# Kernel tuning notes

Measured on AMD Instinct MI355X. Metric: run time of the kernel, lower is better.

## Reference

```python
import jax, jax.numpy as jnp
import numpy as np

B, P, N, E, H, D = 64, 256, 1000, 128, 8, 16
SQRT_E = 11.313708498984761  # sqrt(embedding_dim)
CLIP = 10.0                  # logit_clipping


def setup_inputs() -> dict:
    key = jax.random.key(0)
    ks = jax.random.split(key, 9)
    s = 0.05  # weight init scale
    return {
        "encoded_nodes": jax.random.normal(ks[0], (B, N, E), jnp.float32),
        "encoded_last_node": jax.random.normal(ks[1], (B, P, E), jnp.float32),
        "attr": jax.random.uniform(ks[2], (B, P, 1), jnp.float32),
        "ninf_mask": jnp.zeros((B, P, N), jnp.float32),
        # params stored [in, out] (apply as x @ W, equals torch Linear with W.T)
        "Wq_last": jax.random.normal(ks[3], (E + 1, H * D), jnp.float32) * s,
        "Wk": jax.random.normal(ks[4], (E, H * D), jnp.float32) * s,
        "Wv": jax.random.normal(ks[5], (E, H * D), jnp.float32) * s,
        "Wo": jax.random.normal(ks[6], (H * D, E), jnp.float32) * s,
        "bo": jax.random.normal(ks[7], (E,), jnp.float32) * s,
    }


def reference(encoded_nodes, encoded_last_node, attr, ninf_mask,
              Wq_last, Wk, Wv, Wo, bo):
    # set_kv: project encoded nodes to per-head K, V  -> [B, N, H, D]
    k = (encoded_nodes @ Wk).reshape(B, N, H, D)
    v = (encoded_nodes @ Wv).reshape(B, N, H, D)

    # query from (last node embedding, attr) -> [B, P, H, D]
    input_cat = jnp.concatenate([encoded_last_node, attr], axis=2)  # [B,P,E+1]
    q = (input_cat @ Wq_last).reshape(B, P, H, D)

    # multi-head attention with additive rank-3 -inf mask
    inv_sqrt_d = 1.0 / jnp.sqrt(jnp.float32(D))
    scores = jnp.einsum("bphd,bnhd->bhpn", q, k) * inv_sqrt_d
    scores = scores + ninf_mask[:, None, :, :]            # [B,H,P,N]
    weights = jax.nn.softmax(scores, axis=-1)
    out = jnp.einsum("bhpn,bnhd->bphd", weights, v).reshape(B, P, H * D)

    mh = out @ Wo + bo                                    # [B,P,E]

    # single-head tanh-clipped scoring against encoded nodes
    score = jnp.einsum("bpe,bne->bpn", mh, encoded_nodes) / SQRT_E
    score_masked = CLIP * jnp.tanh(score) + ninf_mask
    probs = jax.nn.softmax(score_masked, axis=2)          # [B,P,N]
    return probs
```

## Files before the change

### kernel.cpp

```cpp
#include <hip/hip_runtime.h>

#define BB 64
#define PP 256
#define NN 1000
#define NP 1024
#define EE 128
#define HH 8
#define DD 16

typedef __fp16 v4h __attribute__((ext_vector_type(4)));
typedef float v4f __attribute__((ext_vector_type(4)));


__global__ __launch_bounds__(256) void k1_qproj(const float* __restrict__ ln,
                                                const float* __restrict__ attr,
                                                const float* __restrict__ Wq,
                                                __fp16* __restrict__ Qh) {
    __shared__ __fp16 wt[128 * 132];
    __shared__ float attrs[64];
    const int tid = threadIdx.x;
    const int row0 = blockIdx.x * 64;
    for (int i = tid; i < 128 * 128; i += 256) {
        int k = i >> 7, n = i & 127;
        wt[n * 132 + k] = (__fp16)Wq[i];
    }
    if (tid < 64) attrs[tid] = attr[row0 + tid];
    __syncthreads();

    const int wid = tid >> 6, lane = tid & 63;
    const int lp = lane & 15, lg = lane >> 4;
    const int rb = row0 + wid * 16;

    const float* arow = ln + (size_t)(rb + lp) * 128;
    v4f acc[8];
#pragma unroll
    for (int cf = 0; cf < 8; cf++) acc[cf] = (v4f){0.f, 0.f, 0.f, 0.f};

#pragma unroll
    for (int k0 = 0; k0 < 8; k0++) {
        float4 av = *(const float4*)&arow[k0 * 16 + 4 * lg];
        v4h af;
        af[0] = (__fp16)av.x; af[1] = (__fp16)av.y;
        af[2] = (__fp16)av.z; af[3] = (__fp16)av.w;
#pragma unroll
        for (int cf = 0; cf < 8; cf++) {
            v4h bf = *(const v4h*)&wt[(cf * 16 + lp) * 132 + k0 * 16 + 4 * lg];
            acc[cf] = __builtin_amdgcn_mfma_f32_16x16x16f16(af, bf, acc[cf], 0, 0, 0);
        }
    }

#pragma unroll
    for (int cf = 0; cf < 8; cf++) {
        const int col = cf * 16 + lp;
        const float w128 = Wq[128 * 128 + col];
#pragma unroll
        for (int r = 0; r < 4; r++) {
            const int rl = wid * 16 + 4 * lg + r;
            float v = (acc[cf][r] + attrs[rl] * w128) * 0.25f;
            Qh[(size_t)(row0 + rl) * 128 + col] = (__fp16)v;
        }
    }
}

__global__ __launch_bounds__(256) void k2_kv(const float* __restrict__ nodes,
                                             const float* __restrict__ Wk,
                                             const float* __restrict__ Wv,
                                             __fp16* __restrict__ Kf,
                                             __fp16* __restrict__ Vf) {
    __shared__ __fp16 wt[128 * 132];
    const int tid = threadIdx.x;
    const int b = blockIdx.y;
    const int kv = blockIdx.z;
    const float* W = (kv == 0) ? Wk : Wv;
    for (int i = tid; i < 128 * 128; i += 256) {
        int k = i >> 7, n = i & 127;
        wt[n * 132 + k] = (__fp16)W[i];
    }
    __syncthreads();

    const int wid = tid >> 6, lane = tid & 63;
    const int lp = lane & 15, lg = lane >> 4;
    const int nb = blockIdx.x * 64 + wid * 16;

    int nr = nb + lp;
    if (nr >= NN) nr = NN - 1;
    const float* arow = nodes + (size_t)(b * NN + nr) * 128;

    v4f acc[8];
#pragma unroll
    for (int cf = 0; cf < 8; cf++) acc[cf] = (v4f){0.f, 0.f, 0.f, 0.f};

#pragma unroll
    for (int k0 = 0; k0 < 8; k0++) {
        float4 av = *(const float4*)&arow[k0 * 16 + 4 * lg];
        v4h af;
        af[0] = (__fp16)av.x; af[1] = (__fp16)av.y;
        af[2] = (__fp16)av.z; af[3] = (__fp16)av.w;
#pragma unroll
        for (int cf = 0; cf < 8; cf++) {
            v4h bf = *(const v4h*)&wt[(cf * 16 + lp) * 132 + k0 * 16 + 4 * lg];
            acc[cf] = __builtin_amdgcn_mfma_f32_16x16x16f16(af, bf, acc[cf], 0, 0, 0);
        }
    }

    if (kv == 0) {
#pragma unroll
        for (int cf = 0; cf < 8; cf++) {
            const size_t base = ((size_t)(b * HH + cf) << 14) + lp;
#pragma unroll
            for (int r = 0; r < 4; r++) {
                const int n = nb + 4 * lg + r;
                Kf[base + (size_t)n * 16] = (n < NN) ? (__fp16)acc[cf][r] : (__fp16)0.f;
            }
        }
    } else {
#pragma unroll
        for (int cf = 0; cf < 8; cf++) {
            v4h pk;
#pragma unroll
            for (int r = 0; r < 4; r++) {
                const int n = nb + 4 * lg + r;
                pk[r] = (n < NN) ? (__fp16)acc[cf][r] : (__fp16)0.f;
            }
            *(v4h*)&Vf[(((size_t)(b * HH + cf) * 16 + lp) << 10) + nb + 4 * lg] = pk;
        }
    }
}

__global__ __launch_bounds__(256, 2) void k3_attn(const __fp16* __restrict__ Qh,
                                                  const __fp16* __restrict__ Kf,
                                                  const __fp16* __restrict__ Vf,
                                                  const float* __restrict__ mask,
                                                  float* __restrict__ Aout) {
    const int tid = threadIdx.x;
    const int bid = blockIdx.x;
    const int rr = bid >> 3;
    const int b = (bid & 7) + ((rr & 7) << 3);
    const int c = rr >> 3;
    const int hg = c & 1, pt = c >> 1;
    const int h0 = hg * 4;
    const int p0 = pt * 64;

    const int wid = tid >> 6, lane = tid & 63;
    const int lp = lane & 15, lg = lane >> 4;
    const int pw = p0 + wid * 16;

    v4h qf[4];
    {
        const __fp16* qrow = Qh + (size_t)(b * PP + pw + lp) * 128 + h0 * 16 + 4 * lg;
#pragma unroll
        for (int j = 0; j < 4; j++) qf[j] = *(const v4h*)&qrow[j * 16];
    }

    v4f acc[4];
    float lsum[4];
#pragma unroll
    for (int j = 0; j < 4; j++) { acc[j] = (v4f){0.f, 0.f, 0.f, 0.f}; lsum[j] = 0.f; }
    const v4f zero4 = {0.f, 0.f, 0.f, 0.f};

    const __fp16* kp = Kf + ((size_t)(b * HH + h0) << 14);
    const __fp16* vp = Vf + ((size_t)((b * HH + h0) * 16) << 10);
    const float* mrow = mask + (size_t)(b * PP + pw + lp) * NN;

#pragma unroll 2
    for (int s = 0; s < 62; s++) {
        const int nl = s * 16;
        v4h kf[4], vf[4];
#pragma unroll
        for (int j = 0; j < 4; j++)
            kf[j] = *(const v4h*)&kp[(j << 14) + (nl + lp) * 16 + 4 * lg];
#pragma unroll
        for (int j = 0; j < 4; j++)
            vf[j] = *(const v4h*)&vp[(j << 14) + lp * NP + nl + 4 * lg];
        float4 mv = *(const float4*)&mrow[nl + 4 * lg];
#pragma unroll
        for (int j = 0; j < 4; j++) {
            v4f sc = __builtin_amdgcn_mfma_f32_16x16x16f16(kf[j], qf[j], zero4, 0, 0, 0);
            float w0 = __expf(sc[0] + mv.x);
            float w1 = __expf(sc[1] + mv.y);
            float w2 = __expf(sc[2] + mv.z);
            float w3 = __expf(sc[3] + mv.w);
            lsum[j] += (w0 + w1) + (w2 + w3);
            v4h wf;
            wf[0] = (__fp16)w0; wf[1] = (__fp16)w1; wf[2] = (__fp16)w2; wf[3] = (__fp16)w3;
            acc[j] = __builtin_amdgcn_mfma_f32_16x16x16f16(wf, vf[j], acc[j], 0, 0, 0);
        }
    }
    {
        const int nl = 992;
        int nc = nl + 4 * lg; if (nc > 996) nc = 996;
        float4 mv = *(const float4*)&mrow[nc];
        const bool b0 = (nl + 4 * lg + 0 < NN), b1 = (nl + 4 * lg + 1 < NN);
        const bool b2 = (nl + 4 * lg + 2 < NN), b3 = (nl + 4 * lg + 3 < NN);
#pragma unroll
        for (int j = 0; j < 4; j++) {
            v4h kf = *(const v4h*)&kp[(j << 14) + (nl + lp) * 16 + 4 * lg];
            v4h vf = *(const v4h*)&vp[(j << 14) + lp * NP + nl + 4 * lg];
            v4f sc = __builtin_amdgcn_mfma_f32_16x16x16f16(kf, qf[j], zero4, 0, 0, 0);
            float w0 = b0 ? __expf(sc[0] + mv.x) : 0.f;
            float w1 = b1 ? __expf(sc[1] + mv.y) : 0.f;
            float w2 = b2 ? __expf(sc[2] + mv.z) : 0.f;
            float w3 = b3 ? __expf(sc[3] + mv.w) : 0.f;
            lsum[j] += (w0 + w1) + (w2 + w3);
            v4h wf;
            wf[0] = (__fp16)w0; wf[1] = (__fp16)w1; wf[2] = (__fp16)w2; wf[3] = (__fp16)w3;
            acc[j] = __builtin_amdgcn_mfma_f32_16x16x16f16(wf, vf, acc[j], 0, 0, 0);
        }
    }

#pragma unroll
    for (int j = 0; j < 4; j++) {
        float l = lsum[j];
        l += __shfl_xor(l, 16);
        l += __shfl_xor(l, 32);
#pragma unroll
        for (int r = 0; r < 4; r++) {
            float denom = __shfl(l, 4 * lg + r);
            float inv = 1.f / denom;
            Aout[(size_t)(b * PP + pw + 4 * lg + r) * 128 + (h0 + j) * 16 + lp] =
                acc[j][r] * inv;
        }
    }
}

__global__ __launch_bounds__(256) void k4_mh(const float* __restrict__ Ain,
                                             const float* __restrict__ Wo,
                                             const float* __restrict__ bo,
                                             __fp16* __restrict__ Mh) {
    __shared__ __fp16 wt[128 * 132];
    const int tid = threadIdx.x;
    const int row0 = blockIdx.x * 64;
    for (int i = tid; i < 128 * 128; i += 256) {
        int k = i >> 7, n = i & 127;
        wt[n * 132 + k] = (__fp16)Wo[i];
    }
    __syncthreads();

    const int wid = tid >> 6, lane = tid & 63;
    const int lp = lane & 15, lg = lane >> 4;
    const int rb = row0 + wid * 16;

    const float* arow = Ain + (size_t)(rb + lp) * 128;
    v4f acc[8];
#pragma unroll
    for (int cf = 0; cf < 8; cf++) acc[cf] = (v4f){0.f, 0.f, 0.f, 0.f};

#pragma unroll
    for (int k0 = 0; k0 < 8; k0++) {
        float4 av = *(const float4*)&arow[k0 * 16 + 4 * lg];
        v4h af;
        af[0] = (__fp16)av.x; af[1] = (__fp16)av.y;
        af[2] = (__fp16)av.z; af[3] = (__fp16)av.w;
#pragma unroll
        for (int cf = 0; cf < 8; cf++) {
            v4h bf = *(const v4h*)&wt[(cf * 16 + lp) * 132 + k0 * 16 + 4 * lg];
            acc[cf] = __builtin_amdgcn_mfma_f32_16x16x16f16(af, bf, acc[cf], 0, 0, 0);
        }
    }

    const float scale = 0.08838834764831845f;
#pragma unroll
    for (int cf = 0; cf < 8; cf++) {
        const int col = cf * 16 + lp;
        const float bb = bo[col];
#pragma unroll
        for (int r = 0; r < 4; r++) {
            const int rl = wid * 16 + 4 * lg + r;
            Mh[(size_t)(row0 + rl) * 128 + col] = (__fp16)((acc[cf][r] + bb) * scale);
        }
    }
}

__global__ __launch_bounds__(256) void k5_final(const float* __restrict__ nodes,
                                                const __fp16* __restrict__ Mh,
                                                const float* __restrict__ mask,
                                                float* __restrict__ out) {
    __shared__ __fp16 probs[16 * 1028];
    __shared__ float rowsum[16];
    __shared__ float rowinv[16];
    const int tid = threadIdx.x;
    const int bid = blockIdx.x;
    const int xcd = bid & 7;
    const int rest = bid >> 3;
    const int pt = rest & 15;
    const int b = ((rest >> 4) << 3) + xcd;
    const int p0 = pt * 16;

    if (tid < 16) rowsum[tid] = 0.f;

    const int wid = tid >> 6, lane = tid & 63;
    const int lp = lane & 15, lg = lane >> 4;

    v4h bf[8];
    {
        const __fp16* mhrow = Mh + (size_t)(b * PP + p0 + lp) * 128;
#pragma unroll
        for (int ec = 0; ec < 8; ec++)
            bf[ec] = *(const v4h*)&mhrow[ec * 16 + 4 * lg];
    }
    __syncthreads();

    float lsum = 0.f;
    const float* nbase = nodes + (size_t)b * NN * 128;
    const float* mkrow = mask + (size_t)(b * PP + p0 + lp) * NN;
    const v4f zero4 = {0.f, 0.f, 0.f, 0.f};

    for (int s = 0; s < 16; s++) {
        const int nt = s * 64 + wid * 16;
        int nr = nt + lp;
        if (nr >= NN) nr = NN - 1;
        const float* arow = nbase + (size_t)nr * 128;
        v4f acc = zero4;
#pragma unroll
        for (int ec = 0; ec < 8; ec++) {
            float4 av = *(const float4*)&arow[ec * 16 + 4 * lg];
            v4h af;
            af[0] = (__fp16)av.x; af[1] = (__fp16)av.y;
            af[2] = (__fp16)av.z; af[3] = (__fp16)av.w;
            acc = __builtin_amdgcn_mfma_f32_16x16x16f16(af, bf[ec], acc, 0, 0, 0);
        }
        const int nb4 = nt + 4 * lg;
        v4h wf;
        if (nt + 15 < NN) {
            float4 mkv = *(const float4*)&mkrow[nb4];
            float e0 = __expf(2.f * acc[0]);
            float e1 = __expf(2.f * acc[1]);
            float e2 = __expf(2.f * acc[2]);
            float e3 = __expf(2.f * acc[3]);
            float w0 = __expf(fmaf(-20.f, __builtin_amdgcn_rcpf(e0 + 1.f), mkv.x));
            float w1 = __expf(fmaf(-20.f, __builtin_amdgcn_rcpf(e1 + 1.f), mkv.y));
            float w2 = __expf(fmaf(-20.f, __builtin_amdgcn_rcpf(e2 + 1.f), mkv.z));
            float w3 = __expf(fmaf(-20.f, __builtin_amdgcn_rcpf(e3 + 1.f), mkv.w));
            lsum += (w0 + w1) + (w2 + w3);
            wf[0] = (__fp16)w0; wf[1] = (__fp16)w1; wf[2] = (__fp16)w2; wf[3] = (__fp16)w3;
        } else {
            float w[4];
#pragma unroll
            for (int r = 0; r < 4; r++) {
                if (nb4 + r < NN) {
                    float e = __expf(2.f * acc[r]);
                    w[r] = __expf(fmaf(-20.f, __builtin_amdgcn_rcpf(e + 1.f),
                                       mkrow[nb4 + r]));
                } else {
                    w[r] = 0.f;
                }
            }
            lsum += (w[0] + w[1]) + (w[2] + w[3]);
            wf[0] = (__fp16)w[0]; wf[1] = (__fp16)w[1];
            wf[2] = (__fp16)w[2]; wf[3] = (__fp16)w[3];
        }
        *(v4h*)&probs[lp * 1028 + nb4] = wf;
    }

    lsum += __shfl_xor(lsum, 16);
    lsum += __shfl_xor(lsum, 32);
    if (lane < 16) atomicAdd(&rowsum[lane], lsum);
    __syncthreads();
    if (tid < 16) rowinv[tid] = 1.f / rowsum[tid];
    __syncthreads();

    if (tid < 250) {
        const int c4 = tid * 4;
        const size_t obase = (size_t)(b * PP + p0) * NN;
#pragma unroll 4
        for (int r = 0; r < 16; r++) {
            v4h pv = *(const v4h*)&probs[r * 1028 + c4];
            float inv = rowinv[r];
            float4 ov;
            ov.x = (float)pv[0] * inv;
            ov.y = (float)pv[1] * inv;
            ov.z = (float)pv[2] * inv;
            ov.w = (float)pv[3] * inv;
            *(float4*)&out[obase + (size_t)r * NN + c4] = ov;
        }
    }
}

extern "C" void kernel_launch(void* const* d_in, const int* in_sizes, int n_in,
                              void* d_out, int out_size, void* d_ws, size_t ws_size,
                              hipStream_t stream) {
    const float* nodes = (const float*)d_in[0];
    const float* ln    = (const float*)d_in[1];
    const float* attr  = (const float*)d_in[2];
    const float* mask  = (const float*)d_in[3];
    const float* Wq    = (const float*)d_in[4];
    const float* Wk    = (const float*)d_in[5];
    const float* Wv    = (const float*)d_in[6];
    const float* Wo    = (const float*)d_in[7];
    const float* bo    = (const float*)d_in[8];
    float* out = (float*)d_out;

    float*  Aout = (float*)d_ws;
    __fp16* Qh   = (__fp16*)(Aout + 2097152);
    __fp16* Mhh  = Qh + 2097152;

    __fp16* Kf = (__fp16*)d_out;
    __fp16* Vf = Kf + (size_t)BB * HH * NP * 16;

    hipLaunchKernelGGL(k1_qproj, dim3(256), dim3(256), 0, stream, ln, attr, Wq, Qh);
    hipLaunchKernelGGL(k2_kv, dim3(16, 64, 2), dim3(256), 0, stream, nodes, Wk, Wv, Kf, Vf);
    hipLaunchKernelGGL(k3_attn, dim3(512), dim3(256), 0, stream, Qh, Kf, Vf, mask, Aout);
    hipLaunchKernelGGL(k4_mh, dim3(256), dim3(256), 0, stream, Aout, Wo, bo, Mhh);
    hipLaunchKernelGGL(k5_final, dim3(1024), dim3(256), 0, stream, nodes, Mhh, mask, out);
}
```

Measured before the change: 331.2 us.

## Split attention over node chunks and combine partial results in output projection

The attention kernel now splits the node dimension into four chunks, launching four times as many blocks with a higher occupancy hint. Each block writes a locally normalised fp16 partial output plus its per-head exp-sum. The output-projection kernel reweights and combines the four partials before its MFMA. This targets the low block count of the previous attention launch on a many-CU GPU. In exchange it adds extra partial-result traffic stored in spare output memory, plus an fp16 rounding step on the partials.

```diff
diff --git a/kernel.cpp b/kernel.cpp
--- a/kernel.cpp
+++ b/kernel.cpp
@@ -127,16 +127,18 @@
     }
 }
 
-__global__ __launch_bounds__(256, 2) void k3_attn(const __fp16* __restrict__ Qh,
+__global__ __launch_bounds__(256, 8) void k3_attn(const __fp16* __restrict__ Qh,
                                                   const __fp16* __restrict__ Kf,
                                                   const __fp16* __restrict__ Vf,
                                                   const float* __restrict__ mask,
-                                                  float* __restrict__ Aout) {
+                                                  __fp16* __restrict__ Ah,
+                                                  float* __restrict__ Ls) {
     const int tid = threadIdx.x;
     const int bid = blockIdx.x;
-    const int rr = bid >> 3;
-    const int b = (bid & 7) + ((rr & 7) << 3);
-    const int c = rr >> 3;
+    const int b = bid & 63;
+    const int rest = bid >> 6;
+    const int c = rest & 7;
+    const int chunk = rest >> 3;
     const int hg = c & 1, pt = c >> 1;
     const int h0 = hg * 4;
     const int p0 = pt * 64;
@@ -162,8 +164,11 @@
     const __fp16* vp = Vf + ((size_t)((b * HH + h0) * 16) << 10);
     const float* mrow = mask + (size_t)(b * PP + pw + lp) * NN;
 
+    const int s0 = chunk << 4;
+    const int send = (chunk == 3) ? 62 : s0 + 16;
+
 #pragma unroll 2
-    for (int s = 0; s < 62; s++) {
+    for (int s = s0; s < send; s++) {
         const int nl = s * 16;
         v4h kf[4], vf[4];
 #pragma unroll
@@ -186,7 +191,7 @@
             acc[j] = __builtin_amdgcn_mfma_f32_16x16x16f16(wf, vf[j], acc[j], 0, 0, 0);
         }
     }
-    {
+    if (chunk == 3) {
         const int nl = 992;
         int nc = nl + 4 * lg; if (nc > 996) nc = 996;
         float4 mv = *(const float4*)&mrow[nc];
@@ -208,22 +213,25 @@
         }
     }
 
+    const size_t gbase = (size_t)chunk * (BB * PP) + (size_t)b * PP + pw;
 #pragma unroll
     for (int j = 0; j < 4; j++) {
         float l = lsum[j];
         l += __shfl_xor(l, 16);
         l += __shfl_xor(l, 32);
+        if (lg == 0) Ls[(gbase + lp) * HH + h0 + j] = l;
 #pragma unroll
         for (int r = 0; r < 4; r++) {
             float denom = __shfl(l, 4 * lg + r);
-            float inv = 1.f / denom;
-            Aout[(size_t)(b * PP + pw + 4 * lg + r) * 128 + (h0 + j) * 16 + lp] =
-                acc[j][r] * inv;
-        }
-    }
-}
-
-__global__ __launch_bounds__(256) void k4_mh(const float* __restrict__ Ain,
+            float inv = (denom > 0.f) ? 1.f / denom : 0.f;
+            Ah[(gbase + 4 * lg + r) * 128 + (h0 + j) * 16 + lp] =
+                (__fp16)(acc[j][r] * inv);
+        }
+    }
+}
+
+__global__ __launch_bounds__(256) void k4_mh(const __fp16* __restrict__ Ah,
+                                             const float* __restrict__ Ls,
                                              const float* __restrict__ Wo,
                                              const float* __restrict__ bo,
                                              __fp16* __restrict__ Mh) {
@@ -239,18 +247,49 @@
     const int wid = tid >> 6, lane = tid & 63;
     const int lp = lane & 15, lg = lane >> 4;
     const int rb = row0 + wid * 16;
-
-    const float* arow = Ain + (size_t)(rb + lp) * 128;
+    const int g = rb + lp;
+
+    float wgt[4][8];
+    {
+        float l[4][8];
+#pragma unroll
+        for (int cc = 0; cc < 4; cc++) {
+            const float* lr = Ls + ((size_t)cc * (BB * PP) + g) * HH;
+            float4 x = *(const float4*)lr;
+            float4 y = *(const float4*)(lr + 4);
+            l[cc][0] = x.x; l[cc][1] = x.y; l[cc][2] = x.z; l[cc][3] = x.w;
+            l[cc][4] = y.x; l[cc][5] = y.y; l[cc][6] = y.z; l[cc][7] = y.w;
+        }
+#pragma unroll
+        for (int h = 0; h < 8; h++) {
+            float s = (l[0][h] + l[1][h]) + (l[2][h] + l[3][h]);
+            float inv = (s > 0.f) ? 1.f / s : 0.f;
+#pragma unroll
+            for (int cc = 0; cc < 4; cc++) wgt[cc][h] = l[cc][h] * inv;
+        }
+    }
+
+    const __fp16* arow = Ah + (size_t)g * 128;
+    const size_t CSTR = (size_t)(BB * PP) * 128;
+
     v4f acc[8];
 #pragma unroll
     for (int cf = 0; cf < 8; cf++) acc[cf] = (v4f){0.f, 0.f, 0.f, 0.f};
 
 #pragma unroll
     for (int k0 = 0; k0 < 8; k0++) {
-        float4 av = *(const float4*)&arow[k0 * 16 + 4 * lg];
+        const int off = k0 * 16 + 4 * lg;
+        v4h p0v = *(const v4h*)&arow[off];
+        v4h p1v = *(const v4h*)&arow[CSTR + off];
+        v4h p2v = *(const v4h*)&arow[2 * CSTR + off];
+        v4h p3v = *(const v4h*)&arow[3 * CSTR + off];
         v4h af;
-        af[0] = (__fp16)av.x; af[1] = (__fp16)av.y;
-        af[2] = (__fp16)av.z; af[3] = (__fp16)av.w;
+#pragma unroll
+        for (int e = 0; e < 4; e++) {
+            float v = (float)p0v[e] * wgt[0][k0] + (float)p1v[e] * wgt[1][k0]
+                    + (float)p2v[e] * wgt[2][k0] + (float)p3v[e] * wgt[3][k0];
+            af[e] = (__fp16)v;
+        }
 #pragma unroll
         for (int cf = 0; cf < 8; cf++) {
             v4h bf = *(const v4h*)&wt[(cf * 16 + lp) * 132 + k0 * 16 + 4 * lg];
@@ -390,16 +429,17 @@
     const float* bo    = (const float*)d_in[8];
     float* out = (float*)d_out;
 
-    float*  Aout = (float*)d_ws;
-    __fp16* Qh   = (__fp16*)(Aout + 2097152);
-    __fp16* Mhh  = Qh + 2097152;
+    __fp16* Qh  = (__fp16*)d_ws;
+    __fp16* Mhh = Qh + 2097152;
 
     __fp16* Kf = (__fp16*)d_out;
     __fp16* Vf = Kf + (size_t)BB * HH * NP * 16;
+    __fp16* Ah = Vf + (size_t)BB * HH * 16 * NP;
+    float*  Ls = (float*)(Ah + (size_t)4 * BB * PP * 128);
 
     hipLaunchKernelGGL(k1_qproj, dim3(256), dim3(256), 0, stream, ln, attr, Wq, Qh);
     hipLaunchKernelGGL(k2_kv, dim3(16, 64, 2), dim3(256), 0, stream, nodes, Wk, Wv, Kf, Vf);
-    hipLaunchKernelGGL(k3_attn, dim3(512), dim3(256), 0, stream, Qh, Kf, Vf, mask, Aout);
-    hipLaunchKernelGGL(k4_mh, dim3(256), dim3(256), 0, stream, Aout, Wo, bo, Mhh);
+    hipLaunchKernelGGL(k3_attn, dim3(2048), dim3(256), 0, stream, Qh, Kf, Vf, mask, Ah, Ls);
+    hipLaunchKernelGGL(k4_mh, dim3(256), dim3(256), 0, stream, Ah, Ls, Wo, bo, Mhh);
     hipLaunchKernelGGL(k5_final, dim3(1024), dim3(256), 0, stream, nodes, Mhh, mask, out);
 }
```

Result: slower. 362.9 us (+9.6%).
